# Performance work log

Measured on AMD Instinct MI355X. Metric: run time of the kernel, lower is better.

## Reference

```python
import jax, jax.numpy as jnp
import numpy as np

N = 50000   # nodes
E = 600000  # edges
H = 128     # hidden_dim


def _linear_params(key, fan_in, fan_out):
    kw, kb = jax.random.split(key)
    s = 1.0 / np.sqrt(fan_in)
    w = jax.random.uniform(kw, (fan_in, fan_out), minval=-s, maxval=s, dtype=jnp.float32)
    b = jax.random.uniform(kb, (fan_out,), minval=-s, maxval=s, dtype=jnp.float32)
    return w, b


def setup_inputs():
    key = jax.random.key(0)
    ks = jax.random.split(key, 9)
    x = jax.random.uniform(ks[0], (N, 1), dtype=jnp.float32)
    pre_h = jax.random.normal(ks[1], (N, H), dtype=jnp.float32)
    edge_index = jax.random.randint(ks[2], (2, E), 0, N, dtype=jnp.int32)
    edge_attr = jax.random.uniform(ks[3], (E, 1), dtype=jnp.float32)
    enc_w, enc_b = _linear_params(ks[4], 1 + H, H)      # BFS_Encoder.linear
    M_w, M_b = _linear_params(ks[5], H + H + 1, H)      # MPNN_Processor.M
    U_w, U_b = _linear_params(ks[6], H + H, H)          # MPNN_Processor.U
    dec_w, dec_b = _linear_params(ks[7], H + H, 1)      # BFS_Decoder.linear
    ter_w, ter_b = _linear_params(ks[8], H + H, 1)      # BFS_Terminator.linear
    return {"x": x, "pre_h": pre_h, "edge_attr": edge_attr,
            "enc_w": enc_w, "enc_b": enc_b, "M_w": M_w, "M_b": M_b,
            "U_w": U_w, "U_b": U_b, "dec_w": dec_w, "dec_b": dec_b,
            "ter_w": ter_w, "ter_b": ter_b, "edge_index": edge_index}


def reference(x, pre_h, edge_attr, enc_w, enc_b, M_w, M_b, U_w, U_b,
              dec_w, dec_b, ter_w, ter_b, edge_index):
    # Encoder: z = relu(Linear([x, pre_h]))
    z = jax.nn.relu(jnp.concatenate([x, pre_h], axis=-1) @ enc_w + enc_b)  # [N,H]

    # Processor (PyG MessagePassing, flow source_to_target):
    # z_i = z[edge_index[1]] (target), z_j = z[edge_index[0]] (source)
    src, tgt = edge_index[0], edge_index[1]
    m = jax.nn.relu(
        jnp.concatenate([z[tgt], z[src], edge_attr], axis=-1) @ M_w + M_b)  # [E,H]
    # scatter-max aggregate into target nodes; empty segments -> 0
    agg = jax.ops.segment_max(m, tgt, num_segments=N)
    agg = jnp.where(jnp.isfinite(agg), agg, 0.0)
    h = jax.nn.relu(jnp.concatenate([z, agg], axis=-1) @ U_w + U_b)  # [N,H]

    # Decoder
    y = jax.nn.sigmoid(jnp.concatenate([z, h], axis=-1) @ dec_w + dec_b)  # [N,1]

    # Terminator: mean over nodes, broadcast-concat, scalar mean
    h_mean = jnp.broadcast_to(jnp.mean(h, axis=0), h.shape)
    ter = jnp.mean(jnp.concatenate([h, h_mean], axis=-1) @ ter_w + ter_b)
    return h, y, ter
```

## Files before the change

kernel.cpp:

```cpp
#include <hip/hip_runtime.h>
#include <hip/hip_bf16.h>
#include <math.h>

#define HD 128
#define APAD 136

typedef short bf16x8 __attribute__((ext_vector_type(8)));
typedef float f32x4 __attribute__((ext_vector_type(4)));

static __device__ __forceinline__ unsigned short f2bf(float f) {
  __hip_bfloat16 b = __float2bfloat16(f);
  return *(unsigned short*)&b;
}
static __device__ __forceinline__ float bflo(unsigned int u) {
  return __uint_as_float(u << 16);
}
static __device__ __forceinline__ float bfhi(unsigned int u) {
  return __uint_as_float(u & 0xffff0000u);
}

__global__ __launch_bounds__(256) void k_frag_hist(
    const float* __restrict__ enc_w, const float* __restrict__ M_w,
    const float* __restrict__ U_w,
    unsigned short* __restrict__ encf, unsigned short* __restrict__ Pf,
    unsigned short* __restrict__ Qf, unsigned short* __restrict__ Uf,
    const int* __restrict__ ei, int* __restrict__ cnt, int E) {
  const int b = blockIdx.x;
  if (b >= 40) {
    const int e = (b - 40) * 256 + threadIdx.x;
    if (e < E) atomicAdd(&cnt[ei[E + e]], 1);
    return;
  }
  const float* W; unsigned short* F; int KS; int lb;
  if (b < 8)       { W = enc_w + HD;     F = encf; KS = 4; lb = b; }
  else if (b < 16) { W = M_w;            F = Pf;   KS = 4; lb = b - 8; }
  else if (b < 24) { W = M_w + HD * HD;  F = Qf;   KS = 4; lb = b - 16; }
  else             { W = U_w;            F = Uf;   KS = 8; lb = b - 24; }
  const int gid = lb * 256 + threadIdx.x;
  const int lane = gid & 63;
  const int ks = (gid >> 6) % KS;
  const int tile = gid / (64 * KS);
  const int col = tile * 16 + (lane & 15);
  const int k0 = ks * 32 + (lane >> 4) * 8;
  unsigned short v[8];
#pragma unroll
  for (int j = 0; j < 8; ++j) v[j] = f2bf(W[(size_t)(k0 + j) * HD + col]);
  unsigned short* dst = F + ((size_t)(tile * KS + ks) * 64 + lane) * 8;
#pragma unroll
  for (int j = 0; j < 8; ++j) dst[j] = v[j];
}

__global__ __launch_bounds__(256) void k_scan_block(
    const int* __restrict__ cnt, int* __restrict__ row_ptr,
    int* __restrict__ partials, int N) {
  __shared__ int s[256];
  const int t = threadIdx.x;
  const int base = blockIdx.x * 1024 + t * 4;
  int v[4], sum = 0;
#pragma unroll
  for (int i = 0; i < 4; ++i) {
    v[i] = (base + i < N) ? cnt[base + i] : 0;
    sum += v[i];
  }
  s[t] = sum;
  __syncthreads();
  for (int off = 1; off < 256; off <<= 1) {
    int xv = (t >= off) ? s[t - off] : 0;
    __syncthreads();
    if (t >= off) s[t] += xv;
    __syncthreads();
  }
  int run = s[t] - sum;
  if (t == 255) partials[blockIdx.x] = s[255];
#pragma unroll
  for (int i = 0; i < 4; ++i) {
    if (base + i < N) row_ptr[base + i] = run;
    run += v[i];
  }
}

__global__ void k_scan_partials(int* __restrict__ partials, int nb) {
  if (threadIdx.x == 0) {
    int run = 0;
    for (int i = 0; i < nb; ++i) { int v = partials[i]; partials[i] = run; run += v; }
  }
}

__global__ __launch_bounds__(256) void k_scan_add(
    int* __restrict__ row_ptr, const int* __restrict__ partials,
    int* __restrict__ cursor, int N) {
  const int base = blockIdx.x * 1024 + threadIdx.x * 4;
  const int p = partials[blockIdx.x];
#pragma unroll
  for (int i = 0; i < 4; ++i) {
    if (base + i < N) {
      int v = row_ptr[base + i] + p;
      row_ptr[base + i] = v;
      cursor[base + i] = v;
    }
  }
}

__global__ __launch_bounds__(256) void k_scatter(
    const int* __restrict__ ei, const float* __restrict__ edge_attr,
    int* __restrict__ cursor, int2* __restrict__ epack, int E) {
  const int e = blockIdx.x * 256 + threadIdx.x;
  if (e >= E) return;
  const int tgt = ei[E + e];
  const int pos = atomicAdd(&cursor[tgt], 1);
  epack[pos] = make_int2(ei[e], __float_as_int(edge_attr[e]));
}

__global__ __launch_bounds__(256, 4) void k_enc_pq(
    const float* __restrict__ x, const float* __restrict__ pre_h,
    const float* __restrict__ enc_w, const float* __restrict__ enc_b,
    const float* __restrict__ M_b,
    const unsigned short* __restrict__ encf, const unsigned short* __restrict__ Pf,
    const unsigned short* __restrict__ Qf,
    unsigned short* __restrict__ zg, unsigned short* __restrict__ Pg,
    unsigned short* __restrict__ Qg) {
  __shared__ unsigned short phs[16 * APAD];
  __shared__ unsigned short zsh[16 * APAD];
  __shared__ float xs[16];
  const int t = threadIdx.x;
  const int n0 = blockIdx.x * 16;

  {
    const int r = t >> 4, c0 = (t & 15) * 8;
    const float4 a = *(const float4*)&pre_h[(size_t)(n0 + r) * HD + c0];
    const float4 b = *(const float4*)&pre_h[(size_t)(n0 + r) * HD + c0 + 4];
    unsigned short* d = &phs[r * APAD + c0];
    d[0] = f2bf(a.x); d[1] = f2bf(a.y); d[2] = f2bf(a.z); d[3] = f2bf(a.w);
    d[4] = f2bf(b.x); d[5] = f2bf(b.y); d[6] = f2bf(b.z); d[7] = f2bf(b.w);
  }
  if (t < 16) xs[t] = x[n0 + t];
  __syncthreads();

  const int w = t >> 6, l = t & 63;
  const int m = l & 15, q = l >> 4;

  bf16x8 af[4];
#pragma unroll
  for (int ks = 0; ks < 4; ++ks)
    af[ks] = *(const bf16x8*)&phs[m * APAD + ks * 32 + q * 8];
  f32x4 acc[2] = {{0, 0, 0, 0}, {0, 0, 0, 0}};
#pragma unroll
  for (int tt = 0; tt < 2; ++tt) {
    const int tn = 2 * w + tt;
#pragma unroll
    for (int ks = 0; ks < 4; ++ks) {
      const bf16x8 bf = *(const bf16x8*)&encf[((size_t)(tn * 4 + ks) * 64 + l) * 8];
      acc[tt] = __builtin_amdgcn_mfma_f32_16x16x32_bf16(af[ks], bf, acc[tt], 0, 0, 0);
    }
  }
#pragma unroll
  for (int tt = 0; tt < 2; ++tt) {
    const int col = (2 * w + tt) * 16 + m;
    const float bb = enc_b[col];
    const float w0 = enc_w[col];
#pragma unroll
    for (int r = 0; r < 4; ++r) {
      const int row = q * 4 + r;
      const float zv = fmaxf(acc[tt][r] + bb + xs[row] * w0, 0.0f);
      zsh[row * APAD + col] = f2bf(zv);
    }
  }
  __syncthreads();

  bf16x8 az[4];
#pragma unroll
  for (int ks = 0; ks < 4; ++ks)
    az[ks] = *(const bf16x8*)&zsh[m * APAD + ks * 32 + q * 8];
  {
    const int r = t >> 4, c0 = (t & 15) * 8;
    *(uint4*)&zg[(size_t)(n0 + r) * HD + c0] = *(const uint4*)&zsh[r * APAD + c0];
  }
  __syncthreads();

  f32x4 pacc[2] = {{0, 0, 0, 0}, {0, 0, 0, 0}};
  f32x4 qacc[2] = {{0, 0, 0, 0}, {0, 0, 0, 0}};
#pragma unroll
  for (int tt = 0; tt < 2; ++tt) {
    const int tn = 2 * w + tt;
#pragma unroll
    for (int ks = 0; ks < 4; ++ks) {
      const bf16x8 bp = *(const bf16x8*)&Pf[((size_t)(tn * 4 + ks) * 64 + l) * 8];
      const bf16x8 bq = *(const bf16x8*)&Qf[((size_t)(tn * 4 + ks) * 64 + l) * 8];
      pacc[tt] = __builtin_amdgcn_mfma_f32_16x16x32_bf16(az[ks], bp, pacc[tt], 0, 0, 0);
      qacc[tt] = __builtin_amdgcn_mfma_f32_16x16x32_bf16(az[ks], bq, qacc[tt], 0, 0, 0);
    }
  }
#pragma unroll
  for (int tt = 0; tt < 2; ++tt) {
    const int col = (2 * w + tt) * 16 + m;
    const float mb = M_b[col];
#pragma unroll
    for (int r = 0; r < 4; ++r) {
      const int row = q * 4 + r;
      phs[row * APAD + col] = f2bf(pacc[tt][r] + mb);
      zsh[row * APAD + col] = f2bf(qacc[tt][r]);
    }
  }
  __syncthreads();
  {
    const int r = t >> 4, c0 = (t & 15) * 8;
    *(uint4*)&Pg[(size_t)(n0 + r) * HD + c0] = *(const uint4*)&phs[r * APAD + c0];
    *(uint4*)&Qg[(size_t)(n0 + r) * HD + c0] = *(const uint4*)&zsh[r * APAD + c0];
  }
}

__global__ __launch_bounds__(256, 6) void k_gather(
    const unsigned short* __restrict__ Pg, const unsigned short* __restrict__ Qg,
    const float* __restrict__ w_attr,
    const int* __restrict__ row_ptr, const int* __restrict__ row_end,
    const int2* __restrict__ epack,
    unsigned short* __restrict__ ag, int N) {
  const int t = threadIdx.x;
  const int w = t >> 6, l = t & 63;
  const int g = l >> 4, j = l & 15;
  const int n0 = blockIdx.x * 32;

  float wv[8];
  {
    const float4 wa = *(const float4*)&w_attr[j * 8];
    const float4 wb = *(const float4*)&w_attr[j * 8 + 4];
    wv[0] = wa.x; wv[1] = wa.y; wv[2] = wa.z; wv[3] = wa.w;
    wv[4] = wb.x; wv[5] = wb.y; wv[6] = wb.z; wv[7] = wb.w;
  }

#pragma unroll
  for (int i = 0; i < 2; ++i) {
    const int r = w * 8 + g * 2 + i;
    const int n = n0 + r;
    const int nc = min(n, N - 1);
    const int rs = row_ptr[nc], re = row_end[nc];
    float acc[8];
#pragma unroll
    for (int c = 0; c < 8; ++c) acc[c] = -INFINITY;
    for (int e = rs; e < re; e += 4) {
      int2 pk[4];
#pragma unroll
      for (int u = 0; u < 4; ++u) pk[u] = epack[min(e + u, re - 1)];
      uint4 qv[4];
#pragma unroll
      for (int u = 0; u < 4; ++u)
        qv[u] = *(const uint4*)&Qg[(size_t)pk[u].x * HD + j * 8];
#pragma unroll
      for (int u = 0; u < 4; ++u) {
        const float a = __int_as_float(pk[u].y);
        const unsigned int qq[4] = {qv[u].x, qv[u].y, qv[u].z, qv[u].w};
#pragma unroll
        for (int c = 0; c < 4; ++c) {
          acc[2 * c]     = fmaxf(acc[2 * c],     fmaf(a, wv[2 * c],     bflo(qq[c])));
          acc[2 * c + 1] = fmaxf(acc[2 * c + 1], fmaf(a, wv[2 * c + 1], bfhi(qq[c])));
        }
      }
    }
    if (n < N) {
      float res[8];
      if (re > rs) {
        const uint4 pv = *(const uint4*)&Pg[(size_t)n * HD + j * 8];
        const unsigned int pp[4] = {pv.x, pv.y, pv.z, pv.w};
#pragma unroll
        for (int c = 0; c < 4; ++c) {
          res[2 * c]     = fmaxf(bflo(pp[c]) + acc[2 * c],     0.0f);
          res[2 * c + 1] = fmaxf(bfhi(pp[c]) + acc[2 * c + 1], 0.0f);
        }
      } else {
#pragma unroll
        for (int c = 0; c < 8; ++c) res[c] = 0.0f;
      }
      uint4 st;
      st.x = (unsigned)f2bf(res[0]) | ((unsigned)f2bf(res[1]) << 16);
      st.y = (unsigned)f2bf(res[2]) | ((unsigned)f2bf(res[3]) << 16);
      st.z = (unsigned)f2bf(res[4]) | ((unsigned)f2bf(res[5]) << 16);
      st.w = (unsigned)f2bf(res[6]) | ((unsigned)f2bf(res[7]) << 16);
      *(uint4*)&ag[(size_t)n * HD + j * 8] = st;
    }
  }
}

__global__ __launch_bounds__(256, 4) void k_update(
    const unsigned short* __restrict__ zg, const unsigned short* __restrict__ ag,
    const unsigned short* __restrict__ Uf,
    const float* __restrict__ U_b, const float* __restrict__ dec_w,
    const float* __restrict__ dec_b,
    float* __restrict__ h_out, float* __restrict__ y_out,
    float* __restrict__ hsum, int N) {
  __shared__ unsigned short zsh[32 * APAD];
  __shared__ unsigned short ash[32 * APAD];
  __shared__ float hcol[HD];
  __shared__ float dacc[32];
  __shared__ float pr[32][8];
  const int t = threadIdx.x;
  const int n0 = blockIdx.x * 32;

  {
    const int r = t >> 3, c0 = (t & 7) * 16;
    const int n = min(n0 + r, N - 1);
    *(uint4*)&zsh[r * APAD + c0]     = *(const uint4*)&zg[(size_t)n * HD + c0];
    *(uint4*)&zsh[r * APAD + c0 + 8] = *(const uint4*)&zg[(size_t)n * HD + c0 + 8];
    *(uint4*)&ash[r * APAD + c0]     = *(const uint4*)&ag[(size_t)n * HD + c0];
    *(uint4*)&ash[r * APAD + c0 + 8] = *(const uint4*)&ag[(size_t)n * HD + c0 + 8];
  }
  if (t < 32) dacc[t] = 0.0f;
  if (t < HD) hcol[t] = 0.0f;
  __syncthreads();

  const int w = t >> 6, l = t & 63;

  const int mt = w & 1, nh = w >> 1;
  const int m = mt * 16 + (l & 15), q = l >> 4;
  bf16x8 afz[4], afa[4];
#pragma unroll
  for (int ks = 0; ks < 4; ++ks) {
    afz[ks] = *(const bf16x8*)&zsh[m * APAD + ks * 32 + q * 8];
    afa[ks] = *(const bf16x8*)&ash[m * APAD + ks * 32 + q * 8];
  }
  f32x4 acc4[4] = {{0, 0, 0, 0}, {0, 0, 0, 0}, {0, 0, 0, 0}, {0, 0, 0, 0}};
#pragma unroll
  for (int tt = 0; tt < 4; ++tt) {
    const int tn = nh * 4 + tt;
#pragma unroll
    for (int ks = 0; ks < 8; ++ks) {
      const bf16x8 bf = *(const bf16x8*)&Uf[((size_t)(tn * 8 + ks) * 64 + l) * 8];
      const bf16x8 a = (ks < 4) ? afz[ks] : afa[ks - 4];
      acc4[tt] = __builtin_amdgcn_mfma_f32_16x16x32_bf16(a, bf, acc4[tt], 0, 0, 0);
    }
  }
  float dp[4] = {0.0f, 0.0f, 0.0f, 0.0f};
#pragma unroll
  for (int tt = 0; tt < 4; ++tt) {
    const int col = (nh * 4 + tt) * 16 + (l & 15);
    const float ub = U_b[col];
    const float dw = dec_w[HD + col];
    float s4 = 0.0f;
#pragma unroll
    for (int r = 0; r < 4; ++r) {
      const int rowl = mt * 16 + q * 4 + r;
      const int n = n0 + rowl;
      float hv = fmaxf(acc4[tt][r] + ub, 0.0f);
      if (n < N) h_out[(size_t)n * HD + col] = hv; else hv = 0.0f;
      s4 += hv;
      dp[r] += hv * dw;
    }
    atomicAdd(&hcol[col], s4);
  }
#pragma unroll
  for (int off = 1; off < 16; off <<= 1) {
#pragma unroll
    for (int r = 0; r < 4; ++r) dp[r] += __shfl_xor(dp[r], off);
  }
  if ((l & 15) == 0) {
#pragma unroll
    for (int r = 0; r < 4; ++r) atomicAdd(&dacc[mt * 16 + q * 4 + r], dp[r]);
  }

  {
    const int r2 = t >> 3, s = t & 7;
    float part = 0.0f;
#pragma unroll
    for (int c = 0; c < 8; ++c) {
      const int kk = s * 16 + 2 * c;
      const unsigned int zu = *(const unsigned int*)&zsh[r2 * APAD + kk];
      part += bflo(zu) * dec_w[kk] + bfhi(zu) * dec_w[kk + 1];
    }
    pr[r2][s] = part;
  }
  __syncthreads();

  if (t < HD) atomicAdd(&hsum[t], hcol[t]);
  if (t < 32 && n0 + t < N) {
    float d = dec_b[0] + dacc[t];
#pragma unroll
    for (int s = 0; s < 8; ++s) d += pr[t][s];
    y_out[n0 + t] = 1.0f / (1.0f + expf(-d));
  }
}

__global__ __launch_bounds__(128) void k_ter(
    const float* __restrict__ hsum, const float* __restrict__ ter_w,
    const float* __restrict__ ter_b, float* __restrict__ out, float invN) {
  __shared__ float r2[2];
  const int t = threadIdx.x;
  float v = (hsum[t] * invN) * (ter_w[t] + ter_w[HD + t]);
#pragma unroll
  for (int o = 32; o > 0; o >>= 1) v += __shfl_down(v, o);
  if ((t & 63) == 0) r2[t >> 6] = v;
  __syncthreads();
  if (t == 0) out[0] = r2[0] + r2[1] + ter_b[0];
}

extern "C" void kernel_launch(void* const* d_in, const int* in_sizes, int n_in,
                              void* d_out, int out_size, void* d_ws, size_t ws_size,
                              hipStream_t stream) {
  const float* x        = (const float*)d_in[0];
  const float* pre_h    = (const float*)d_in[1];
  const float* edge_attr= (const float*)d_in[2];
  const float* enc_w    = (const float*)d_in[3];
  const float* enc_b    = (const float*)d_in[4];
  const float* M_w      = (const float*)d_in[5];
  const float* M_b      = (const float*)d_in[6];
  const float* U_w      = (const float*)d_in[7];
  const float* U_b      = (const float*)d_in[8];
  const float* dec_w    = (const float*)d_in[9];
  const float* dec_b    = (const float*)d_in[10];
  const float* ter_w    = (const float*)d_in[11];
  const float* ter_b    = (const float*)d_in[12];
  const int*   edge_idx = (const int*)d_in[13];

  const int N = in_sizes[0];
  const int E = in_sizes[2];
  const size_t NH = (size_t)N * HD;

  float* out = (float*)d_out;
  float* h_out = out;
  float* y_out = out + NH;
  float* ter_out = out + NH + N;

  unsigned short* zg = (unsigned short*)d_ws;
  unsigned short* Pg = zg + NH;
  unsigned short* Qg = Pg + NH;
  unsigned short* ag = Qg + NH;
  int*   cursor   = (int*)(ag + NH);
  int*   row_ptr  = cursor + N;
  int*   partials = row_ptr + N;
  float* hsum     = (float*)(partials + 64);
  int2*  epack    = (int2*)(hsum + HD);
  unsigned short* encf = (unsigned short*)(epack + E);
  unsigned short* Pf   = encf + 8 * 4 * 64 * 8;
  unsigned short* Qf   = Pf + 8 * 4 * 64 * 8;
  unsigned short* Uf   = Qf + 8 * 4 * 64 * 8;

  hipMemsetAsync(cursor, 0, (2 * (size_t)N + 64 + HD) * sizeof(int), stream);

  const int scan_blocks = (N + 1023) / 1024;
  const int eb = (E + 255) / 256;

  k_frag_hist<<<40 + eb, 256, 0, stream>>>(enc_w, M_w, U_w, encf, Pf, Qf, Uf,
                                           edge_idx, cursor, E);
  k_scan_block<<<scan_blocks, 256, 0, stream>>>(cursor, row_ptr, partials, N);
  k_scan_partials<<<1, 64, 0, stream>>>(partials, scan_blocks);
  k_scan_add<<<scan_blocks, 256, 0, stream>>>(row_ptr, partials, cursor, N);
  k_scatter<<<eb, 256, 0, stream>>>(edge_idx, edge_attr, cursor, epack, E);

  k_enc_pq<<<N / 16, 256, 0, stream>>>(x, pre_h, enc_w, enc_b, M_b,
                                       encf, Pf, Qf, zg, Pg, Qg);
  k_gather<<<(N + 31) / 32, 256, 0, stream>>>(
      Pg, Qg, M_w + 256 * HD, row_ptr, cursor, epack, ag, N);
  k_update<<<(N + 31) / 32, 256, 0, stream>>>(
      zg, ag, Uf, U_b, dec_w, dec_b, h_out, y_out, hsum, N);
  k_ter<<<1, 128, 0, stream>>>(hsum, ter_w, ter_b, ter_out, 1.0f / (float)N);
}
```

Before: 274.0 us.

## Fuse gather into update kernel, single-block scan, per-block h partials

Merges the edge gather/max-aggregate kernel into the node update kernel so the aggregated features are written straight to shared memory rather than round-tripping through a global bf16 buffer. The three-kernel prefix scan becomes one 1024-thread single-block scan, and the atomic column sum for the terminator becomes per-block partials reduced by one final kernel. This removes launches, global traffic and atomics. In exchange the fused kernel holds more registers and has less latency hiding, and the single-block scan and reduction run serially on one CU.

Measured after the change: 405.3 us. 1.48x slower.

```diff
diff --git a/kernel.cpp b/kernel.cpp
--- a/kernel.cpp
+++ b/kernel.cpp
@@ -50,53 +50,33 @@
   for (int j = 0; j < 8; ++j) dst[j] = v[j];
 }
 
-__global__ __launch_bounds__(256) void k_scan_block(
-    const int* __restrict__ cnt, int* __restrict__ row_ptr,
-    int* __restrict__ partials, int N) {
-  __shared__ int s[256];
+__global__ __launch_bounds__(1024) void k_scan(
+    int* __restrict__ cursor, int* __restrict__ row_ptr, int N) {
+  __shared__ int s[1024];
   const int t = threadIdx.x;
-  const int base = blockIdx.x * 1024 + t * 4;
-  int v[4], sum = 0;
-#pragma unroll
-  for (int i = 0; i < 4; ++i) {
-    v[i] = (base + i < N) ? cnt[base + i] : 0;
-    sum += v[i];
+  const int C = (N + 1023) >> 10;
+  const int base = t * C;
+  int sum = 0;
+  for (int i = 0; i < C; ++i) {
+    const int idx = base + i;
+    if (idx < N) sum += cursor[idx];
   }
   s[t] = sum;
   __syncthreads();
-  for (int off = 1; off < 256; off <<= 1) {
+  for (int off = 1; off < 1024; off <<= 1) {
     int xv = (t >= off) ? s[t - off] : 0;
     __syncthreads();
     if (t >= off) s[t] += xv;
     __syncthreads();
   }
   int run = s[t] - sum;
-  if (t == 255) partials[blockIdx.x] = s[255];
-#pragma unroll
-  for (int i = 0; i < 4; ++i) {
-    if (base + i < N) row_ptr[base + i] = run;
-    run += v[i];
-  }
-}
-
-__global__ void k_scan_partials(int* __restrict__ partials, int nb) {
-  if (threadIdx.x == 0) {
-    int run = 0;
-    for (int i = 0; i < nb; ++i) { int v = partials[i]; partials[i] = run; run += v; }
-  }
-}
-
-__global__ __launch_bounds__(256) void k_scan_add(
-    int* __restrict__ row_ptr, const int* __restrict__ partials,
-    int* __restrict__ cursor, int N) {
-  const int base = blockIdx.x * 1024 + threadIdx.x * 4;
-  const int p = partials[blockIdx.x];
-#pragma unroll
-  for (int i = 0; i < 4; ++i) {
-    if (base + i < N) {
-      int v = row_ptr[base + i] + p;
-      row_ptr[base + i] = v;
-      cursor[base + i] = v;
+  for (int i = 0; i < C; ++i) {
+    const int idx = base + i;
+    if (idx < N) {
+      const int c = cursor[idx];
+      row_ptr[idx] = run;
+      cursor[idx] = run;
+      run += c;
     }
   }
 }
@@ -209,84 +189,15 @@
   }
 }
 
-__global__ __launch_bounds__(256, 6) void k_gather(
-    const unsigned short* __restrict__ Pg, const unsigned short* __restrict__ Qg,
-    const float* __restrict__ w_attr,
+__global__ __launch_bounds__(256, 6) void k_gu(
+    const unsigned short* __restrict__ zg, const unsigned short* __restrict__ Pg,
+    const unsigned short* __restrict__ Qg, const float* __restrict__ w_attr,
     const int* __restrict__ row_ptr, const int* __restrict__ row_end,
-    const int2* __restrict__ epack,
-    unsigned short* __restrict__ ag, int N) {
-  const int t = threadIdx.x;
-  const int w = t >> 6, l = t & 63;
-  const int g = l >> 4, j = l & 15;
-  const int n0 = blockIdx.x * 32;
-
-  float wv[8];
-  {
-    const float4 wa = *(const float4*)&w_attr[j * 8];
-    const float4 wb = *(const float4*)&w_attr[j * 8 + 4];
-    wv[0] = wa.x; wv[1] = wa.y; wv[2] = wa.z; wv[3] = wa.w;
-    wv[4] = wb.x; wv[5] = wb.y; wv[6] = wb.z; wv[7] = wb.w;
-  }
-
-#pragma unroll
-  for (int i = 0; i < 2; ++i) {
-    const int r = w * 8 + g * 2 + i;
-    const int n = n0 + r;
-    const int nc = min(n, N - 1);
-    const int rs = row_ptr[nc], re = row_end[nc];
-    float acc[8];
-#pragma unroll
-    for (int c = 0; c < 8; ++c) acc[c] = -INFINITY;
-    for (int e = rs; e < re; e += 4) {
-      int2 pk[4];
-#pragma unroll
-      for (int u = 0; u < 4; ++u) pk[u] = epack[min(e + u, re - 1)];
-      uint4 qv[4];
-#pragma unroll
-      for (int u = 0; u < 4; ++u)
-        qv[u] = *(const uint4*)&Qg[(size_t)pk[u].x * HD + j * 8];
-#pragma unroll
-      for (int u = 0; u < 4; ++u) {
-        const float a = __int_as_float(pk[u].y);
-        const unsigned int qq[4] = {qv[u].x, qv[u].y, qv[u].z, qv[u].w};
-#pragma unroll
-        for (int c = 0; c < 4; ++c) {
-          acc[2 * c]     = fmaxf(acc[2 * c],     fmaf(a, wv[2 * c],     bflo(qq[c])));
-          acc[2 * c + 1] = fmaxf(acc[2 * c + 1], fmaf(a, wv[2 * c + 1], bfhi(qq[c])));
-        }
-      }
-    }
-    if (n < N) {
-      float res[8];
-      if (re > rs) {
-        const uint4 pv = *(const uint4*)&Pg[(size_t)n * HD + j * 8];
-        const unsigned int pp[4] = {pv.x, pv.y, pv.z, pv.w};
-#pragma unroll
-        for (int c = 0; c < 4; ++c) {
-          res[2 * c]     = fmaxf(bflo(pp[c]) + acc[2 * c],     0.0f);
-          res[2 * c + 1] = fmaxf(bfhi(pp[c]) + acc[2 * c + 1], 0.0f);
-        }
-      } else {
-#pragma unroll
-        for (int c = 0; c < 8; ++c) res[c] = 0.0f;
-      }
-      uint4 st;
-      st.x = (unsigned)f2bf(res[0]) | ((unsigned)f2bf(res[1]) << 16);
-      st.y = (unsigned)f2bf(res[2]) | ((unsigned)f2bf(res[3]) << 16);
-      st.z = (unsigned)f2bf(res[4]) | ((unsigned)f2bf(res[5]) << 16);
-      st.w = (unsigned)f2bf(res[6]) | ((unsigned)f2bf(res[7]) << 16);
-      *(uint4*)&ag[(size_t)n * HD + j * 8] = st;
-    }
-  }
-}
-
-__global__ __launch_bounds__(256, 4) void k_update(
-    const unsigned short* __restrict__ zg, const unsigned short* __restrict__ ag,
-    const unsigned short* __restrict__ Uf,
+    const int2* __restrict__ epack, const unsigned short* __restrict__ Uf,
     const float* __restrict__ U_b, const float* __restrict__ dec_w,
     const float* __restrict__ dec_b,
     float* __restrict__ h_out, float* __restrict__ y_out,
-    float* __restrict__ hsum, int N) {
+    float* __restrict__ hpart, int N) {
   __shared__ unsigned short zsh[32 * APAD];
   __shared__ unsigned short ash[32 * APAD];
   __shared__ float hcol[HD];
@@ -300,14 +211,69 @@
     const int n = min(n0 + r, N - 1);
     *(uint4*)&zsh[r * APAD + c0]     = *(const uint4*)&zg[(size_t)n * HD + c0];
     *(uint4*)&zsh[r * APAD + c0 + 8] = *(const uint4*)&zg[(size_t)n * HD + c0 + 8];
-    *(uint4*)&ash[r * APAD + c0]     = *(const uint4*)&ag[(size_t)n * HD + c0];
-    *(uint4*)&ash[r * APAD + c0 + 8] = *(const uint4*)&ag[(size_t)n * HD + c0 + 8];
   }
   if (t < 32) dacc[t] = 0.0f;
   if (t < HD) hcol[t] = 0.0f;
-  __syncthreads();
 
   const int w = t >> 6, l = t & 63;
+  const int g = l >> 4, j = l & 15;
+
+  float wv[8];
+  {
+    const float4 wa = *(const float4*)&w_attr[j * 8];
+    const float4 wb = *(const float4*)&w_attr[j * 8 + 4];
+    wv[0] = wa.x; wv[1] = wa.y; wv[2] = wa.z; wv[3] = wa.w;
+    wv[4] = wb.x; wv[5] = wb.y; wv[6] = wb.z; wv[7] = wb.w;
+  }
+#pragma unroll
+  for (int i = 0; i < 2; ++i) {
+    const int r = w * 8 + g * 2 + i;
+    const int n = n0 + r;
+    const int nc = min(n, N - 1);
+    const int rs = row_ptr[nc], re = row_end[nc];
+    float acc[8];
+#pragma unroll
+    for (int c = 0; c < 8; ++c) acc[c] = -INFINITY;
+    for (int e = rs; e < re; e += 4) {
+      int2 pk[4];
+#pragma unroll
+      for (int u = 0; u < 4; ++u) pk[u] = epack[min(e + u, re - 1)];
+      uint4 qv[4];
+#pragma unroll
+      for (int u = 0; u < 4; ++u)
+        qv[u] = *(const uint4*)&Qg[(size_t)pk[u].x * HD + j * 8];
+#pragma unroll
+      for (int u = 0; u < 4; ++u) {
+        const float a = __int_as_float(pk[u].y);
+        const unsigned int qq[4] = {qv[u].x, qv[u].y, qv[u].z, qv[u].w};
+#pragma unroll
+        for (int c = 0; c < 4; ++c) {
+          acc[2 * c]     = fmaxf(acc[2 * c],     fmaf(a, wv[2 * c],     bflo(qq[c])));
+          acc[2 * c + 1] = fmaxf(acc[2 * c + 1], fmaf(a, wv[2 * c + 1], bfhi(qq[c])));
+        }
+      }
+    }
+    float res[8];
+    if (n < N && re > rs) {
+      const uint4 pv = *(const uint4*)&Pg[(size_t)n * HD + j * 8];
+      const unsigned int pp[4] = {pv.x, pv.y, pv.z, pv.w};
+#pragma unroll
+      for (int c = 0; c < 4; ++c) {
+        res[2 * c]     = fmaxf(bflo(pp[c]) + acc[2 * c],     0.0f);
+        res[2 * c + 1] = fmaxf(bfhi(pp[c]) + acc[2 * c + 1], 0.0f);
+      }
+    } else {
+#pragma unroll
+      for (int c = 0; c < 8; ++c) res[c] = 0.0f;
+    }
+    uint4 st;
+    st.x = (unsigned)f2bf(res[0]) | ((unsigned)f2bf(res[1]) << 16);
+    st.y = (unsigned)f2bf(res[2]) | ((unsigned)f2bf(res[3]) << 16);
+    st.z = (unsigned)f2bf(res[4]) | ((unsigned)f2bf(res[5]) << 16);
+    st.w = (unsigned)f2bf(res[6]) | ((unsigned)f2bf(res[7]) << 16);
+    *(uint4*)&ash[r * APAD + j * 8] = st;
+  }
+  __syncthreads();
 
   const int mt = w & 1, nh = w >> 1;
   const int m = mt * 16 + (l & 15), q = l >> 4;
@@ -369,7 +335,7 @@
   }
   __syncthreads();
 
-  if (t < HD) atomicAdd(&hsum[t], hcol[t]);
+  if (t < HD) hpart[(size_t)blockIdx.x * HD + t] = hcol[t];
   if (t < 32 && n0 + t < N) {
     float d = dec_b[0] + dacc[t];
 #pragma unroll
@@ -378,17 +344,33 @@
   }
 }
 
-__global__ __launch_bounds__(128) void k_ter(
-    const float* __restrict__ hsum, const float* __restrict__ ter_w,
-    const float* __restrict__ ter_b, float* __restrict__ out, float invN) {
-  __shared__ float r2[2];
+__global__ __launch_bounds__(1024) void k_hredter(
+    const float* __restrict__ hpart, const float* __restrict__ ter_w,
+    const float* __restrict__ ter_b, float* __restrict__ out,
+    float invN, int NB) {
+  __shared__ float s[1024];
   const int t = threadIdx.x;
-  float v = (hsum[t] * invN) * (ter_w[t] + ter_w[HD + t]);
+  const int col = t & (HD - 1);
+  const int grp = t >> 7;
+  float acc = 0.0f;
+  for (int r = grp; r < NB; r += 8) acc += hpart[(size_t)r * HD + col];
+  s[t] = acc;
+  __syncthreads();
+  if (t < 512) s[t] += s[t + 512];
+  __syncthreads();
+  if (t < 256) s[t] += s[t + 256];
+  __syncthreads();
+  float v = 0.0f;
+  if (t < 128) {
+    const float colsum = s[t] + s[t + 128];
+    v = (colsum * invN) * (ter_w[t] + ter_w[HD + t]);
+  }
 #pragma unroll
   for (int o = 32; o > 0; o >>= 1) v += __shfl_down(v, o);
-  if ((t & 63) == 0) r2[t >> 6] = v;
-  __syncthreads();
-  if (t == 0) out[0] = r2[0] + r2[1] + ter_b[0];
+  __syncthreads();
+  if (t < 128 && (t & 63) == 0) s[t >> 6] = v;
+  __syncthreads();
+  if (t == 0) out[0] = s[0] + s[1] + ter_b[0];
 }
 
 extern "C" void kernel_launch(void* const* d_in, const int* in_sizes, int n_in,
@@ -421,34 +403,29 @@
   unsigned short* zg = (unsigned short*)d_ws;
   unsigned short* Pg = zg + NH;
   unsigned short* Qg = Pg + NH;
-  unsigned short* ag = Qg + NH;
-  int*   cursor   = (int*)(ag + NH);
+  int*   cursor   = (int*)(Qg + NH);
   int*   row_ptr  = cursor + N;
-  int*   partials = row_ptr + N;
-  float* hsum     = (float*)(partials + 64);
-  int2*  epack    = (int2*)(hsum + HD);
+  int2*  epack    = (int2*)(row_ptr + N);
   unsigned short* encf = (unsigned short*)(epack + E);
   unsigned short* Pf   = encf + 8 * 4 * 64 * 8;
   unsigned short* Qf   = Pf + 8 * 4 * 64 * 8;
   unsigned short* Uf   = Qf + 8 * 4 * 64 * 8;
-
-  hipMemsetAsync(cursor, 0, (2 * (size_t)N + 64 + HD) * sizeof(int), stream);
-
-  const int scan_blocks = (N + 1023) / 1024;
+  float* hpart = (float*)(Uf + 16 * 256 * 8);
+
+  hipMemsetAsync(cursor, 0, (size_t)N * sizeof(int), stream);
+
   const int eb = (E + 255) / 256;
+  const int nb32 = (N + 31) / 32;
 
   k_frag_hist<<<40 + eb, 256, 0, stream>>>(enc_w, M_w, U_w, encf, Pf, Qf, Uf,
                                            edge_idx, cursor, E);
-  k_scan_block<<<scan_blocks, 256, 0, stream>>>(cursor, row_ptr, partials, N);
-  k_scan_partials<<<1, 64, 0, stream>>>(partials, scan_blocks);
-  k_scan_add<<<scan_blocks, 256, 0, stream>>>(row_ptr, partials, cursor, N);
+  k_scan<<<1, 1024, 0, stream>>>(cursor, row_ptr, N);
   k_scatter<<<eb, 256, 0, stream>>>(edge_idx, edge_attr, cursor, epack, E);
-
   k_enc_pq<<<N / 16, 256, 0, stream>>>(x, pre_h, enc_w, enc_b, M_b,
                                        encf, Pf, Qf, zg, Pg, Qg);
-  k_gather<<<(N + 31) / 32, 256, 0, stream>>>(
-      Pg, Qg, M_w + 256 * HD, row_ptr, cursor, epack, ag, N);
-  k_update<<<(N + 31) / 32, 256, 0, stream>>>(
-      zg, ag, Uf, U_b, dec_w, dec_b, h_out, y_out, hsum, N);
-  k_ter<<<1, 128, 0, stream>>>(hsum, ter_w, ter_b, ter_out, 1.0f / (float)N);
-}
+  k_gu<<<nb32, 256, 0, stream>>>(
+      zg, Pg, Qg, M_w + 256 * HD, row_ptr, cursor, epack, Uf,
+      U_b, dec_w, dec_b, h_out, y_out, hpart, N);
+  k_hredter<<<1, 1024, 0, stream>>>(hpart, ter_w, ter_b, ter_out,
+                                    1.0f / (float)N, nb32);
+}
```
